# Performance work log

Measured on AMD Instinct MI355X. Metric: run time of the kernel, lower is better.

Reference implementation:

```python
import jax, jax.numpy as jnp
from jax import lax
import numpy as np
import math

NUM_CLASSES = 81
N_PER_IMG = 1024
NUM_IMAGES = 8
SCORE_THRESH = 0.05
NMS_THRESH = 0.5
DETS_PER_IMG = 100
WX, WY, WW, WH = 10.0, 10.0, 5.0, 5.0
BBOX_XFORM_CLIP = math.log(1000.0 / 16.0)


def setup_inputs() -> dict:
    key = jax.random.key(0)
    k1, k2, k3, k4 = jax.random.split(key, 4)
    M = NUM_IMAGES * N_PER_IMG
    H, W = 800, 1333
    class_logits = jax.random.normal(k1, (M, NUM_CLASSES), dtype=jnp.float32) * 3.0
    box_regression = jax.random.normal(k2, (M, 4 * NUM_CLASSES), dtype=jnp.float32) * 0.5
    # valid xyxy proposals inside the image
    xy1 = jax.random.uniform(k3, (M, 2), dtype=jnp.float32) * jnp.array([W * 0.7, H * 0.7], jnp.float32)
    wh = jax.random.uniform(k4, (M, 2), dtype=jnp.float32) * jnp.array([W * 0.3, H * 0.3], jnp.float32) + 4.0
    proposals = jnp.concatenate([xy1, xy1 + wh], axis=1)
    return {"class_logits": class_logits, "box_regression": box_regression,
            "proposals": proposals, "height": H, "width": W}


def _decode(rel_codes, boxes):
    widths = boxes[:, 2] - boxes[:, 0] + 1.0
    heights = boxes[:, 3] - boxes[:, 1] + 1.0
    ctr_x = boxes[:, 0] + 0.5 * widths
    ctr_y = boxes[:, 1] + 0.5 * heights
    rel = rel_codes.reshape(rel_codes.shape[0], -1, 4)  # [M, C, 4]
    dx = rel[:, :, 0] / WX
    dy = rel[:, :, 1] / WY
    dw = jnp.minimum(rel[:, :, 2] / WW, BBOX_XFORM_CLIP)
    dh = jnp.minimum(rel[:, :, 3] / WH, BBOX_XFORM_CLIP)
    pctr_x = dx * widths[:, None] + ctr_x[:, None]
    pctr_y = dy * heights[:, None] + ctr_y[:, None]
    pw = jnp.exp(dw) * widths[:, None]
    ph = jnp.exp(dh) * heights[:, None]
    return jnp.stack([pctr_x - 0.5 * pw, pctr_y - 0.5 * ph,
                      pctr_x + 0.5 * pw - 1.0, pctr_y + 0.5 * ph - 1.0], axis=-1)


def _clip(boxes, height, width):
    # boxes [..., 4] xyxy, clamp to [0, W-1] x [0, H-1]
    x = jnp.clip(boxes[..., 0::2], 0.0, float(width - 1))
    y = jnp.clip(boxes[..., 1::2], 0.0, float(height - 1))
    return jnp.stack([x[..., 0], y[..., 0], x[..., 1], y[..., 1]], axis=-1)


def _iou_matrix(b):
    x1, y1, x2, y2 = b[:, 0], b[:, 1], b[:, 2], b[:, 3]
    area = (x2 - x1 + 1.0) * (y2 - y1 + 1.0)
    xx1 = jnp.maximum(x1[:, None], x1[None, :])
    yy1 = jnp.maximum(y1[:, None], y1[None, :])
    xx2 = jnp.minimum(x2[:, None], x2[None, :])
    yy2 = jnp.minimum(y2[:, None], y2[None, :])
    inter = jnp.clip(xx2 - xx1 + 1.0, 0.0) * jnp.clip(yy2 - yy1 + 1.0, 0.0)
    return inter / (area[:, None] + area[None, :] - inter)


def _per_class(scores_j, boxes_j):
    # scores_j [N], boxes_j [N,4] -> sorted scores/boxes + greedy-NMS keep mask
    N = scores_j.shape[0]
    valid = scores_j > SCORE_THRESH
    s = jnp.where(valid, scores_j, 0.0)  # softmax scores are > 0
    order = jnp.argsort(-s)
    s_sorted = s[order]
    b_sorted = boxes_j[order]
    valid_sorted = valid[order]
    iou = _iou_matrix(b_sorted)  # [N, N]
    idxs = jnp.arange(N)

    def body(i, keep):
        sup = (iou[i] > NMS_THRESH) & keep[i] & (idxs > i)
        return keep & ~sup

    keep = lax.fori_loop(0, N, body, valid_sorted)
    return s_sorted, b_sorted, keep


def _per_image(prob_i, boxes_i):
    # prob_i [N, C], boxes_i [N, C, 4]; skip background class 0
    C = prob_i.shape[1]
    fg_scores = prob_i[:, 1:].T                      # [C-1, N]
    fg_boxes = jnp.swapaxes(boxes_i[:, 1:, :], 0, 1)  # [C-1, N, 4]
    s_sorted, b_sorted, keep = jax.vmap(_per_class)(fg_scores, fg_boxes)
    labels = jnp.broadcast_to(jnp.arange(1, C, dtype=jnp.int32)[:, None], s_sorted.shape)
    flat_s = jnp.where(keep, s_sorted, 0.0).reshape(-1)
    vals, idx = lax.top_k(flat_s, DETS_PER_IMG)      # detections-per-image limit
    boxes_out = b_sorted.reshape(-1, 4)[idx]
    labels_out = labels.reshape(-1)[idx]
    ok = vals > SCORE_THRESH
    return (jnp.where(ok, vals, 0.0),
            jnp.where(ok[:, None], boxes_out, 0.0),
            jnp.where(ok, labels_out, 0))


def reference(class_logits, box_regression, proposals, height, width):
    prob = jax.nn.softmax(class_logits, axis=-1)          # [M, C]
    dec = _decode(box_regression, proposals)              # [M, C, 4]
    dec = _clip(dec, height, width)
    B, N, C = NUM_IMAGES, N_PER_IMG, NUM_CLASSES
    prob = prob.reshape(B, N, C)
    dec = dec.reshape(B, N, C, 4)
    scores, boxes, labels = lax.map(lambda a: _per_image(a[0], a[1]), (prob, dec))
    return scores, boxes, labels
```

## Files before the change

### kernel.cpp

```cpp
#include <hip/hip_runtime.h>
#include <stdint.h>
#include <math.h>

#define NCLS 81
#define NFG  80
#define NPI  1024
#define NIMG 8
#define DETS 100
#define SCORE_T 0.05f
#define NMS_T   0.5f
#define NCAND   (NFG * DETS)
#define CAND_CAP 2048
#define FASTN 256
#define ROWS 64

static constexpr float BBOX_CLIP = 4.1351665567423557f;

__global__ __launch_bounds__(256) void softmax_probT(
    const float* __restrict__ logits, float* __restrict__ probT, int M)
{
    __shared__ float tile[ROWS * NCLS];
    __shared__ float mx[ROWS], dn[ROWS];
    int t = threadIdx.x;
    int rbase = blockIdx.x * ROWS;

    for (int idx = t; idx < ROWS * NCLS; idx += 256)
        tile[idx] = logits[(size_t)rbase * NCLS + idx];
    __syncthreads();

    if (t < ROWS) {
        const float* r = tile + t * NCLS;
        float m = r[0];
        #pragma unroll
        for (int j = 1; j < NCLS; ++j) m = fmaxf(m, r[j]);
        float s = 0.f;
        #pragma unroll
        for (int j = 0; j < NCLS; ++j) s += expf(r[j] - m);
        mx[t] = m; dn[t] = s;
    }
    __syncthreads();

    for (int o = t; o < ROWS * NFG; o += 256) {
        int r = o & 63;
        int c = o >> 6;
        float v = expf(tile[r * NCLS + (c + 1)] - mx[r]) / dn[r];
        probT[(size_t)c * M + rbase + r] = v;
    }
}

__global__ __launch_bounds__(256) void per_class_nms(
    const float* __restrict__ probT, const float* __restrict__ boxreg,
    const float* __restrict__ props, const int* __restrict__ hptr,
    const int* __restrict__ wptr, int* __restrict__ out_cnt,
    float* __restrict__ out_score, unsigned* __restrict__ out_key,
    float* __restrict__ out_box, int M)
{
    int pid = blockIdx.x;
    int img = pid / NFG;
    int c   = pid % NFG;
    int cls = c + 1;

    __shared__ float box_lds[NPI][4];
    __shared__ unsigned long long key[NPI];
    __shared__ int keep[NPI];
    __shared__ float sbox[FASTN][4];
    __shared__ float sarea[FASTN];
    __shared__ unsigned long long mask[FASTN][FASTN/64];
    __shared__ unsigned long long keepw[FASTN/64];
    __shared__ unsigned wpre[4];
    __shared__ int cnt;

    int t = threadIdx.x;
    float W1 = (float)(*wptr - 1);
    float H1 = (float)(*hptr - 1);

    if (t == 0) cnt = 0;
    for (int i = t; i < NPI; i += 256) key[i] = 0ULL;
    __syncthreads();

    {
        const float4 pv = *(const float4*)(probT + (size_t)c * M + img * NPI + 4 * t);
        float pr[4] = {pv.x, pv.y, pv.z, pv.w};
        #pragma unroll
        for (int j = 0; j < 4; ++j) {
            if (pr[j] > SCORE_T) {
                int m = 4 * t + j;
                int g = img * NPI + m;
                const float4 pb = *(const float4*)(props + (size_t)g * 4);
                float x1 = pb.x, y1 = pb.y, x2 = pb.z, y2 = pb.w;
                float w  = x2 - x1 + 1.0f, h = y2 - y1 + 1.0f;
                float cx = x1 + 0.5f * w,  cy = y1 + 0.5f * h;
                const float4 rc = *(const float4*)(boxreg + (size_t)g * (4 * NCLS) + 4 * cls);
                float dx = rc.x / 10.0f, dy = rc.y / 10.0f;
                float dw = fminf(rc.z / 5.0f, BBOX_CLIP);
                float dh = fminf(rc.w / 5.0f, BBOX_CLIP);
                float pcx = dx * w + cx, pcy = dy * h + cy;
                float pw = expf(dw) * w, ph = expf(dh) * h;
                float bx1 = pcx - 0.5f * pw;
                float by1 = pcy - 0.5f * ph;
                float bx2 = pcx + 0.5f * pw - 1.0f;
                float by2 = pcy + 0.5f * ph - 1.0f;
                bx1 = fminf(fmaxf(bx1, 0.f), W1);
                bx2 = fminf(fmaxf(bx2, 0.f), W1);
                by1 = fminf(fmaxf(by1, 0.f), H1);
                by2 = fminf(fmaxf(by2, 0.f), H1);
                box_lds[m][0] = bx1; box_lds[m][1] = by1;
                box_lds[m][2] = bx2; box_lds[m][3] = by2;
                int p = atomicAdd(&cnt, 1);
                unsigned fb = __float_as_uint(pr[j]);
                key[p] = ((unsigned long long)fb << 32) | (unsigned)(NPI - 1 - m);
            }
        }
    }
    __syncthreads();
    int n = cnt;

    if (n <= 64) {
        if (t < 64) {
            int lane = t;
            unsigned long long k = (lane < n) ? key[lane] : 0ULL;
            #pragma unroll
            for (int kk = 2; kk <= 64; kk <<= 1) {
                #pragma unroll
                for (int j = kk >> 1; j > 0; j >>= 1) {
                    unsigned long long o = __shfl_xor(k, j, 64);
                    bool up = ((lane & kk) == 0);
                    bool lower = ((lane & j) == 0);
                    bool take_max = (up == lower);
                    k = take_max ? (k > o ? k : o) : (k < o ? k : o);
                }
            }
            bool valid = (lane < n);
            float bx1 = 0.f, by1 = 0.f, bx2 = 0.f, by2 = 0.f, area = 0.f;
            if (valid) {
                int mi = NPI - 1 - (int)(k & 0xFFFFFFFFu);
                bx1 = box_lds[mi][0]; by1 = box_lds[mi][1];
                bx2 = box_lds[mi][2]; by2 = box_lds[mi][3];
                area = (bx2 - bx1 + 1.f) * (by2 - by1 + 1.f);
            }
            unsigned long long sup = 0ULL;
            for (int i = 0; i < n; ++i) {
                bool alive = !((sup >> i) & 1ULL);
                float ax1 = __shfl(bx1, i, 64), ay1 = __shfl(by1, i, 64);
                float ax2 = __shfl(bx2, i, 64), ay2 = __shfl(by2, i, 64);
                float aarea = __shfl(area, i, 64);
                bool s = false;
                if (alive && valid && lane > i) {
                    float xx1 = fmaxf(ax1, bx1), yy1 = fmaxf(ay1, by1);
                    float xx2 = fminf(ax2, bx2), yy2 = fminf(ay2, by2);
                    float iw = fmaxf(xx2 - xx1 + 1.f, 0.f);
                    float ih = fmaxf(yy2 - yy1 + 1.f, 0.f);
                    float inter = iw * ih;
                    float iou = inter / (aarea + area - inter);
                    s = iou > NMS_T;
                }
                sup |= __ballot(s);
            }
            bool kept = valid && !((sup >> lane) & 1ULL);
            unsigned long long keptm = __ballot(kept);
            int rank = __popcll(keptm & ((1ULL << lane) - 1ULL));
            if (kept && rank < DETS) {
                int slot = pid * DETS + rank;
                out_score[slot] = __uint_as_float((unsigned)(k >> 32));
                out_key[slot] = (unsigned)(c * NPI + lane);
                out_box[slot * 4 + 0] = bx1;
                out_box[slot * 4 + 1] = by1;
                out_box[slot * 4 + 2] = bx2;
                out_box[slot * 4 + 3] = by2;
            }
            if (lane == 0) {
                int tot = __popcll(keptm);
                out_cnt[pid] = tot < DETS ? tot : DETS;
            }
        }
        return;
    }

    int P = 2;
    while (P < n) P <<= 1;
    for (int k = 2; k <= P; k <<= 1) {
        for (int j = k >> 1; j > 0; j >>= 1) {
            for (int i = t; i < P; i += 256) {
                int ixj = i ^ j;
                if (ixj > i) {
                    unsigned long long a = key[i], b = key[ixj];
                    bool up = (i & k) == 0;
                    if (up ? (a < b) : (a > b)) { key[i] = b; key[ixj] = a; }
                }
            }
            __syncthreads();
        }
    }

    for (int i = t; i < NPI; i += 256) keep[i] = 0;
    __syncthreads();

    if (n <= FASTN) {
        for (int i = t; i < n; i += 256) {
            int mi = NPI - 1 - (int)(key[i] & 0xFFFFFFFFu);
            float bx1 = box_lds[mi][0], by1 = box_lds[mi][1];
            float bx2 = box_lds[mi][2], by2 = box_lds[mi][3];
            sbox[i][0] = bx1; sbox[i][1] = by1; sbox[i][2] = bx2; sbox[i][3] = by2;
            sarea[i] = (bx2 - bx1 + 1.f) * (by2 - by1 + 1.f);
        }
        __syncthreads();
        int nwords = ((n + 63) >> 6);
        for (int w = t; w < n * (FASTN/64); w += 256) {
            int i = w >> 2, wb = w & 3;
            if (wb >= nwords || ((wb + 1) << 6) - 1 <= i) { mask[i][wb] = 0ULL; continue; }
            float ax1 = sbox[i][0], ay1 = sbox[i][1];
            float ax2 = sbox[i][2], ay2 = sbox[i][3];
            float aarea = sarea[i];
            unsigned long long bits = 0ULL;
            int jbase = wb << 6;
            #pragma unroll 4
            for (int b = 0; b < 64; ++b) {
                int j = jbase + b;
                if (j < n && j > i) {
                    float bx1 = sbox[j][0], by1 = sbox[j][1];
                    float bx2 = sbox[j][2], by2 = sbox[j][3];
                    float xx1 = fmaxf(ax1, bx1), yy1 = fmaxf(ay1, by1);
                    float xx2 = fminf(ax2, bx2), yy2 = fminf(ay2, by2);
                    float iw = fmaxf(xx2 - xx1 + 1.f, 0.f);
                    float ih = fmaxf(yy2 - yy1 + 1.f, 0.f);
                    float inter = iw * ih;
                    float iou = inter / (aarea + sarea[j] - inter);
                    if (iou > NMS_T) bits |= (1ULL << b);
                }
            }
            mask[i][wb] = bits;
        }
        __syncthreads();
        if (t < 64) {
            int lane = t;
            unsigned long long kb = 0ULL;
            if (lane < 4) {
                int rem = n - (lane << 6);
                if (rem >= 64) kb = ~0ULL;
                else if (rem > 0) kb = (1ULL << rem) - 1ULL;
            }
            unsigned long long rm = 0ULL;
            for (int i = 0; i < n; ++i) {
                unsigned long long rw = __shfl(rm, i >> 6, 64);
                if (!((rw >> (i & 63)) & 1ULL)) {
                    unsigned long long mrow = (lane < 4) ? mask[i][lane] : 0ULL;
                    rm |= mrow;
                }
            }
            if (lane < 4) keepw[lane] = kb & ~rm;
        }
        __syncthreads();
        for (int i = t; i < n; i += 256)
            keep[i] = (int)((keepw[i >> 6] >> (i & 63)) & 1ULL);
        __syncthreads();
    } else {
        for (int i = t; i < n; i += 256) keep[i] = 1;
        __syncthreads();
        for (int i = 0; i < n; ++i) {
            if (keep[i]) {
                unsigned long long ki = key[i];
                int mi = NPI - 1 - (int)(ki & 0xFFFFFFFFu);
                float ax1 = box_lds[mi][0], ay1 = box_lds[mi][1];
                float ax2 = box_lds[mi][2], ay2 = box_lds[mi][3];
                float aarea = (ax2 - ax1 + 1.f) * (ay2 - ay1 + 1.f);
                for (int jj = i + 1 + t; jj < n; jj += 256) {
                    if (keep[jj]) {
                        int mj = NPI - 1 - (int)(key[jj] & 0xFFFFFFFFu);
                        float bx1 = box_lds[mj][0], by1 = box_lds[mj][1];
                        float bx2 = box_lds[mj][2], by2 = box_lds[mj][3];
                        float xx1 = fmaxf(ax1, bx1), yy1 = fmaxf(ay1, by1);
                        float xx2 = fminf(ax2, bx2), yy2 = fminf(ay2, by2);
                        float iw = fmaxf(xx2 - xx1 + 1.f, 0.f);
                        float ih = fmaxf(yy2 - yy1 + 1.f, 0.f);
                        float inter = iw * ih;
                        float barea = (bx2 - bx1 + 1.f) * (by2 - by1 + 1.f);
                        float iou = inter / (aarea + barea - inter);
                        if (iou > NMS_T) keep[jj] = 0;
                    }
                }
            }
            __syncthreads();
        }
    }

    {
        int lane = t & 63, w = t >> 6;
        int k0 = keep[4 * t], k1 = keep[4 * t + 1];
        int k2 = keep[4 * t + 2], k3 = keep[4 * t + 3];
        unsigned s = (unsigned)(k0 + k1 + k2 + k3);
        unsigned v = s;
        #pragma unroll
        for (int off = 1; off < 64; off <<= 1) {
            unsigned u = __shfl_up(v, off, 64);
            v += (lane >= off) ? u : 0u;
        }
        if (lane == 63) wpre[w] = v;
        __syncthreads();
        unsigned woff = 0;
        for (int w2 = 0; w2 < w; ++w2) woff += wpre[w2];
        unsigned before = v + woff - s;
        unsigned r = before;
        #pragma unroll
        for (int j = 0; j < 4; ++j) {
            int i = 4 * t + j;
            int kv = (j == 0) ? k0 : (j == 1) ? k1 : (j == 2) ? k2 : k3;
            if (kv && r < DETS) {
                unsigned long long ki = key[i];
                int mi = NPI - 1 - (int)(ki & 0xFFFFFFFFu);
                int slot = pid * DETS + (int)r;
                out_score[slot] = __uint_as_float((unsigned)(ki >> 32));
                out_key[slot] = (unsigned)(c * NPI + i);
                out_box[slot * 4 + 0] = box_lds[mi][0];
                out_box[slot * 4 + 1] = box_lds[mi][1];
                out_box[slot * 4 + 2] = box_lds[mi][2];
                out_box[slot * 4 + 3] = box_lds[mi][3];
            }
            r += (unsigned)kv;
        }
        __syncthreads();
        if (t == 0) {
            unsigned tot = wpre[0] + wpre[1] + wpre[2] + wpre[3];
            out_cnt[pid] = (int)(tot < DETS ? tot : DETS);
        }
    }
}

__device__ __forceinline__ void suffix_select(
    unsigned* hist, unsigned* wtot, int K, int* outB, unsigned* outAbove)
{
    int t = threadIdx.x, lane = t & 63, w = t >> 6;
    unsigned c0 = hist[4 * t], c1 = hist[4 * t + 1];
    unsigned c2 = hist[4 * t + 2], c3 = hist[4 * t + 3];
    unsigned ps = c0 + c1 + c2 + c3;
    unsigned v = ps;
    #pragma unroll
    for (int off = 1; off < 64; off <<= 1) {
        unsigned u = __shfl_down(v, off, 64);
        v += (lane + off < 64) ? u : 0u;
    }
    if (lane == 0) wtot[w] = v;
    __syncthreads();
    unsigned woff = 0;
    for (int w2 = w + 1; w2 < 16; ++w2) woff += wtot[w2];
    unsigned Sown = v + woff;
    unsigned A3 = Sown - ps;
    unsigned A2 = A3 + c3, A1 = A2 + c2, A0 = A1 + c1;
    unsigned A[4] = {A0, A1, A2, A3};
    unsigned C[4] = {c0, c1, c2, c3};
    #pragma unroll
    for (int j = 0; j < 4; ++j) {
        if ((int)A[j] < K && (int)(A[j] + C[j]) >= K) {
            *outB = 4 * t + j;
            *outAbove = A[j];
        }
    }
    __syncthreads();
}

__global__ __launch_bounds__(1024) void topk_merge(
    const int* __restrict__ cnts, const float* __restrict__ escore,
    const unsigned* __restrict__ ekey, const float* __restrict__ ebox,
    float* __restrict__ out)
{
    int img = blockIdx.x;
    __shared__ unsigned sc[NCAND];
    __shared__ unsigned hist[4096];
    __shared__ unsigned long long cand[CAND_CAP];
    __shared__ unsigned wtot[16];
    __shared__ int sB1, sB2, sNc;
    __shared__ unsigned sAb1, sAb2;

    int t = threadIdx.x;
    if (t == 0) { sB1 = 0; sB2 = 0; sNc = 0; sAb1 = 0; sAb2 = 0; }
    for (int p = t; p < NCAND; p += 1024) {
        int cc = p / DETS, k = p % DETS;
        unsigned fb = 0;
        if (k < cnts[img * NFG + cc]) fb = __float_as_uint(escore[img * NCAND + p]);
        sc[p] = fb;
    }
    for (int i = t; i < 4096; i += 1024) hist[i] = 0;
    __syncthreads();

    for (int p = t; p < NCAND; p += 1024) {
        unsigned fb = sc[p];
        if (fb) atomicAdd(&hist[fb >> 19], 1u);
    }
    __syncthreads();
    suffix_select(hist, wtot, DETS, &sB1, &sAb1);
    int B1 = sB1;
    unsigned ab1 = sAb1;

    for (int i = t; i < 4096; i += 1024) hist[i] = 0;
    __syncthreads();
    for (int p = t; p < NCAND; p += 1024) {
        unsigned fb = sc[p];
        if (fb && (int)(fb >> 19) == B1) atomicAdd(&hist[(fb >> 7) & 0xFFFu], 1u);
    }
    __syncthreads();
    suffix_select(hist, wtot, DETS - (int)ab1, &sB2, &sAb2);
    int B2 = sB2;

    for (int p = t; p < NCAND; p += 1024) {
        unsigned fb = sc[p];
        if (fb) {
            int d1 = (int)(fb >> 19);
            bool ok = d1 > B1 || (d1 == B1 && (int)((fb >> 7) & 0xFFFu) >= B2);
            if (ok) {
                int pos = atomicAdd(&sNc, 1);
                if (pos < CAND_CAP) {
                    unsigned fk = ekey[img * NCAND + p];
                    unsigned low = ((0x1FFFFu - fk) << 13) | (unsigned)p;
                    cand[pos] = ((unsigned long long)fb << 32) | low;
                }
            }
        }
    }
    __syncthreads();
    int nc = sNc < CAND_CAP ? sNc : CAND_CAP;
    int P = 128;
    while (P < nc) P <<= 1;
    for (int i = t; i < P; i += 1024)
        if (i >= nc) cand[i] = 0ULL;
    __syncthreads();

    for (int k = 2; k <= P; k <<= 1) {
        for (int j = k >> 1; j > 0; j >>= 1) {
            for (int i = t; i < P; i += 1024) {
                int ixj = i ^ j;
                if (ixj > i) {
                    unsigned long long a = cand[i], b = cand[ixj];
                    bool up = (i & k) == 0;
                    if (up ? (a < b) : (a > b)) { cand[i] = b; cand[ixj] = a; }
                }
            }
            __syncthreads();
        }
    }

    float* oScore = out;
    float* oBox   = out + NIMG * DETS;
    float* oLab   = out + NIMG * DETS * 5;

    if (t < DETS) {
        unsigned long long b = cand[t];
        int o = img * DETS + t;
        if (b != 0ULL) {
            float scv = __uint_as_float((unsigned)(b >> 32));
            unsigned low = (unsigned)(b & 0xFFFFFFFFu);
            unsigned flatkey = 0x1FFFFu - ((low >> 13) & 0x1FFFFu);
            int p = (int)(low & 0x1FFFu);
            int gp = img * NCAND + p;
            oScore[o] = scv;
            oBox[o * 4 + 0] = ebox[gp * 4 + 0];
            oBox[o * 4 + 1] = ebox[gp * 4 + 1];
            oBox[o * 4 + 2] = ebox[gp * 4 + 2];
            oBox[o * 4 + 3] = ebox[gp * 4 + 3];
            oLab[o] = (float)((flatkey >> 10) + 1);
        } else {
            oScore[o] = 0.f;
            oBox[o * 4 + 0] = 0.f; oBox[o * 4 + 1] = 0.f;
            oBox[o * 4 + 2] = 0.f; oBox[o * 4 + 3] = 0.f;
            oLab[o] = 0.f;
        }
    }
}

extern "C" void kernel_launch(void* const* d_in, const int* in_sizes, int n_in,
                              void* d_out, int out_size, void* d_ws, size_t ws_size,
                              hipStream_t stream) {
    const float* logits = (const float*)d_in[0];
    const float* boxreg = (const float*)d_in[1];
    const float* props  = (const float*)d_in[2];
    const int*   hptr   = (const int*)d_in[3];
    const int*   wptr   = (const int*)d_in[4];
    float* out = (float*)d_out;
    int M = in_sizes[0] / NCLS;

    char* ws = (char*)d_ws;
    float*    probT  = (float*)ws;    ws += (size_t)NFG * M * sizeof(float);
    int*      cnt    = (int*)ws;      ws += (size_t)NIMG * NFG * sizeof(int);
    float*    escore = (float*)ws;    ws += (size_t)NIMG * NCAND * sizeof(float);
    unsigned* ekey   = (unsigned*)ws; ws += (size_t)NIMG * NCAND * sizeof(unsigned);
    float*    ebox   = (float*)ws;    ws += (size_t)NIMG * NCAND * 4 * sizeof(float);

    softmax_probT<<<M / ROWS, 256, 0, stream>>>(logits, probT, M);
    per_class_nms<<<NIMG * NFG, 256, 0, stream>>>(
        probT, boxreg, props, hptr, wptr, cnt, escore, ekey, ebox, M);
    topk_merge<<<NIMG, 1024, 0, stream>>>(cnt, escore, ekey, ebox, out);
}
```

Before: 61.07 us.

## Fuse top-k merge into NMS kernel via last-block completion counter

Replaces the transposed probability materialization with a per-row max/denominator stats kernel, so the NMS kernel computes class probabilities directly from the logits. The separate top-k merge launch is folded into the NMS kernel: the last block to finish each image, detected with an atomic counter, performs the merge in 256 threads using shared memory unioned with the NMS buffers. This removes one launch and the probT write and read, at the cost of strided logit reads, a serial tail where one 256-thread block merges each image, and reliance on the stats kernel resetting the done counters.

```diff
diff --git a/kernel.cpp b/kernel.cpp
--- a/kernel.cpp
+++ b/kernel.cpp
@@ -16,433 +16,123 @@
 
 static constexpr float BBOX_CLIP = 4.1351665567423557f;
 
-__global__ __launch_bounds__(256) void softmax_probT(
-    const float* __restrict__ logits, float* __restrict__ probT, int M)
+struct ShP2 {
+    float box[NPI][4];
+    unsigned long long key[NPI];
+    int keep[NPI];
+    float sbox[FASTN][4];
+    float sarea[FASTN];
+    unsigned long long mask[FASTN][FASTN/64];
+    unsigned long long keepw[FASTN/64];
+    unsigned wpre[4];
+};
+struct ShP3 {
+    unsigned hist[4096];
+    unsigned long long cand[CAND_CAP];
+    int cnts[NFG];
+    unsigned wtot[4];
+    int B1, B2, Nc;
+    unsigned Ab1, Ab2;
+};
+union ShU { ShP2 p2; ShP3 p3; };
+
+__device__ __forceinline__ void suffix_select256(
+    unsigned* hist, unsigned* wtot, int K, int* outB, unsigned* outAbove)
 {
-    __shared__ float tile[ROWS * NCLS];
-    __shared__ float mx[ROWS], dn[ROWS];
+    int t = threadIdx.x, lane = t & 63, w = t >> 6;
+    unsigned loc[16]; unsigned ps = 0;
+    #pragma unroll
+    for (int j = 0; j < 16; ++j) { loc[j] = hist[t * 16 + j]; ps += loc[j]; }
+    unsigned v = ps;
+    #pragma unroll
+    for (int off = 1; off < 64; off <<= 1) {
+        unsigned u = __shfl_down(v, off, 64);
+        v += (lane + off < 64) ? u : 0u;
+    }
+    if (lane == 0) wtot[w] = v;
+    __syncthreads();
+    unsigned woff = 0;
+    for (int w2 = w + 1; w2 < 4; ++w2) woff += wtot[w2];
+    unsigned base = v + woff - ps;
+    unsigned suf = 0;
+    #pragma unroll
+    for (int j = 15; j >= 0; --j) {
+        unsigned A = base + suf;
+        if ((int)A < K && (int)(A + loc[j]) >= K) { *outB = t * 16 + j; *outAbove = A; }
+        suf += loc[j];
+    }
+    __syncthreads();
+}
+
+__device__ void merge_image(
+    int img, ShP3& s3, const int* gcnt, const float* escore,
+    const unsigned* ekey, const float* ebox, float* out)
+{
     int t = threadIdx.x;
-    int rbase = blockIdx.x * ROWS;
-
-    for (int idx = t; idx < ROWS * NCLS; idx += 256)
-        tile[idx] = logits[(size_t)rbase * NCLS + idx];
-    __syncthreads();
-
-    if (t < ROWS) {
-        const float* r = tile + t * NCLS;
-        float m = r[0];
-        #pragma unroll
-        for (int j = 1; j < NCLS; ++j) m = fmaxf(m, r[j]);
-        float s = 0.f;
-        #pragma unroll
-        for (int j = 0; j < NCLS; ++j) s += expf(r[j] - m);
-        mx[t] = m; dn[t] = s;
-    }
-    __syncthreads();
-
-    for (int o = t; o < ROWS * NFG; o += 256) {
-        int r = o & 63;
-        int c = o >> 6;
-        float v = expf(tile[r * NCLS + (c + 1)] - mx[r]) / dn[r];
-        probT[(size_t)c * M + rbase + r] = v;
-    }
-}
-
-__global__ __launch_bounds__(256) void per_class_nms(
-    const float* __restrict__ probT, const float* __restrict__ boxreg,
-    const float* __restrict__ props, const int* __restrict__ hptr,
-    const int* __restrict__ wptr, int* __restrict__ out_cnt,
-    float* __restrict__ out_score, unsigned* __restrict__ out_key,
-    float* __restrict__ out_box, int M)
-{
-    int pid = blockIdx.x;
-    int img = pid / NFG;
-    int c   = pid % NFG;
-    int cls = c + 1;
-
-    __shared__ float box_lds[NPI][4];
-    __shared__ unsigned long long key[NPI];
-    __shared__ int keep[NPI];
-    __shared__ float sbox[FASTN][4];
-    __shared__ float sarea[FASTN];
-    __shared__ unsigned long long mask[FASTN][FASTN/64];
-    __shared__ unsigned long long keepw[FASTN/64];
-    __shared__ unsigned wpre[4];
-    __shared__ int cnt;
-
-    int t = threadIdx.x;
-    float W1 = (float)(*wptr - 1);
-    float H1 = (float)(*hptr - 1);
-
-    if (t == 0) cnt = 0;
-    for (int i = t; i < NPI; i += 256) key[i] = 0ULL;
-    __syncthreads();
-
-    {
-        const float4 pv = *(const float4*)(probT + (size_t)c * M + img * NPI + 4 * t);
-        float pr[4] = {pv.x, pv.y, pv.z, pv.w};
-        #pragma unroll
-        for (int j = 0; j < 4; ++j) {
-            if (pr[j] > SCORE_T) {
-                int m = 4 * t + j;
-                int g = img * NPI + m;
-                const float4 pb = *(const float4*)(props + (size_t)g * 4);
-                float x1 = pb.x, y1 = pb.y, x2 = pb.z, y2 = pb.w;
-                float w  = x2 - x1 + 1.0f, h = y2 - y1 + 1.0f;
-                float cx = x1 + 0.5f * w,  cy = y1 + 0.5f * h;
-                const float4 rc = *(const float4*)(boxreg + (size_t)g * (4 * NCLS) + 4 * cls);
-                float dx = rc.x / 10.0f, dy = rc.y / 10.0f;
-                float dw = fminf(rc.z / 5.0f, BBOX_CLIP);
-                float dh = fminf(rc.w / 5.0f, BBOX_CLIP);
-                float pcx = dx * w + cx, pcy = dy * h + cy;
-                float pw = expf(dw) * w, ph = expf(dh) * h;
-                float bx1 = pcx - 0.5f * pw;
-                float by1 = pcy - 0.5f * ph;
-                float bx2 = pcx + 0.5f * pw - 1.0f;
-                float by2 = pcy + 0.5f * ph - 1.0f;
-                bx1 = fminf(fmaxf(bx1, 0.f), W1);
-                bx2 = fminf(fmaxf(bx2, 0.f), W1);
-                by1 = fminf(fmaxf(by1, 0.f), H1);
-                by2 = fminf(fmaxf(by2, 0.f), H1);
-                box_lds[m][0] = bx1; box_lds[m][1] = by1;
-                box_lds[m][2] = bx2; box_lds[m][3] = by2;
-                int p = atomicAdd(&cnt, 1);
-                unsigned fb = __float_as_uint(pr[j]);
-                key[p] = ((unsigned long long)fb << 32) | (unsigned)(NPI - 1 - m);
-            }
-        }
-    }
-    __syncthreads();
-    int n = cnt;
-
-    if (n <= 64) {
-        if (t < 64) {
-            int lane = t;
-            unsigned long long k = (lane < n) ? key[lane] : 0ULL;
-            #pragma unroll
-            for (int kk = 2; kk <= 64; kk <<= 1) {
-                #pragma unroll
-                for (int j = kk >> 1; j > 0; j >>= 1) {
-                    unsigned long long o = __shfl_xor(k, j, 64);
-                    bool up = ((lane & kk) == 0);
-                    bool lower = ((lane & j) == 0);
-                    bool take_max = (up == lower);
-                    k = take_max ? (k > o ? k : o) : (k < o ? k : o);
-                }
-            }
-            bool valid = (lane < n);
-            float bx1 = 0.f, by1 = 0.f, bx2 = 0.f, by2 = 0.f, area = 0.f;
-            if (valid) {
-                int mi = NPI - 1 - (int)(k & 0xFFFFFFFFu);
-                bx1 = box_lds[mi][0]; by1 = box_lds[mi][1];
-                bx2 = box_lds[mi][2]; by2 = box_lds[mi][3];
-                area = (bx2 - bx1 + 1.f) * (by2 - by1 + 1.f);
-            }
-            unsigned long long sup = 0ULL;
-            for (int i = 0; i < n; ++i) {
-                bool alive = !((sup >> i) & 1ULL);
-                float ax1 = __shfl(bx1, i, 64), ay1 = __shfl(by1, i, 64);
-                float ax2 = __shfl(bx2, i, 64), ay2 = __shfl(by2, i, 64);
-                float aarea = __shfl(area, i, 64);
-                bool s = false;
-                if (alive && valid && lane > i) {
-                    float xx1 = fmaxf(ax1, bx1), yy1 = fmaxf(ay1, by1);
-                    float xx2 = fminf(ax2, bx2), yy2 = fminf(ay2, by2);
-                    float iw = fmaxf(xx2 - xx1 + 1.f, 0.f);
-                    float ih = fmaxf(yy2 - yy1 + 1.f, 0.f);
-                    float inter = iw * ih;
-                    float iou = inter / (aarea + area - inter);
-                    s = iou > NMS_T;
-                }
-                sup |= __ballot(s);
-            }
-            bool kept = valid && !((sup >> lane) & 1ULL);
-            unsigned long long keptm = __ballot(kept);
-            int rank = __popcll(keptm & ((1ULL << lane) - 1ULL));
-            if (kept && rank < DETS) {
-                int slot = pid * DETS + rank;
-                out_score[slot] = __uint_as_float((unsigned)(k >> 32));
-                out_key[slot] = (unsigned)(c * NPI + lane);
-                out_box[slot * 4 + 0] = bx1;
-                out_box[slot * 4 + 1] = by1;
-                out_box[slot * 4 + 2] = bx2;
-                out_box[slot * 4 + 3] = by2;
-            }
-            if (lane == 0) {
-                int tot = __popcll(keptm);
-                out_cnt[pid] = tot < DETS ? tot : DETS;
-            }
-        }
-        return;
-    }
-
-    int P = 2;
-    while (P < n) P <<= 1;
+    if (t < NFG) s3.cnts[t] = gcnt[img * NFG + t];
+    if (t == 0) { s3.B1 = 0; s3.B2 = 0; s3.Nc = 0; s3.Ab1 = 0; s3.Ab2 = 0; }
+    for (int i = t; i < 4096; i += 256) s3.hist[i] = 0;
+    __syncthreads();
+    for (int p = t; p < NCAND; p += 256) {
+        if ((p % DETS) < s3.cnts[p / DETS]) {
+            unsigned fb = __float_as_uint(escore[img * NCAND + p]);
+            atomicAdd(&s3.hist[fb >> 19], 1u);
+        }
+    }
+    __syncthreads();
+    suffix_select256(s3.hist, s3.wtot, DETS, &s3.B1, &s3.Ab1);
+    int B1 = s3.B1; unsigned ab1 = s3.Ab1;
+    for (int i = t; i < 4096; i += 256) s3.hist[i] = 0;
+    __syncthreads();
+    for (int p = t; p < NCAND; p += 256) {
+        if ((p % DETS) < s3.cnts[p / DETS]) {
+            unsigned fb = __float_as_uint(escore[img * NCAND + p]);
+            if ((int)(fb >> 19) == B1) atomicAdd(&s3.hist[(fb >> 7) & 0xFFFu], 1u);
+        }
+    }
+    __syncthreads();
+    suffix_select256(s3.hist, s3.wtot, DETS - (int)ab1, &s3.B2, &s3.Ab2);
+    int B2 = s3.B2;
+    for (int p = t; p < NCAND; p += 256) {
+        if ((p % DETS) < s3.cnts[p / DETS]) {
+            unsigned fb = __float_as_uint(escore[img * NCAND + p]);
+            int d1 = (int)(fb >> 19);
+            bool ok = d1 > B1 || (d1 == B1 && (int)((fb >> 7) & 0xFFFu) >= B2);
+            if (ok) {
+                int pos = atomicAdd(&s3.Nc, 1);
+                if (pos < CAND_CAP) {
+                    unsigned fk = ekey[img * NCAND + p];
+                    s3.cand[pos] = ((unsigned long long)fb << 32)
+                                 | (((0x1FFFFu - fk) << 13) | (unsigned)p);
+                }
+            }
+        }
+    }
+    __syncthreads();
+    int nc = s3.Nc < CAND_CAP ? s3.Nc : CAND_CAP;
+    int P = 128;
+    while (P < nc) P <<= 1;
+    for (int i = t; i < P; i += 256)
+        if (i >= nc) s3.cand[i] = 0ULL;
+    __syncthreads();
     for (int k = 2; k <= P; k <<= 1) {
         for (int j = k >> 1; j > 0; j >>= 1) {
             for (int i = t; i < P; i += 256) {
                 int ixj = i ^ j;
                 if (ixj > i) {
-                    unsigned long long a = key[i], b = key[ixj];
+                    unsigned long long a = s3.cand[i], b = s3.cand[ixj];
                     bool up = (i & k) == 0;
-                    if (up ? (a < b) : (a > b)) { key[i] = b; key[ixj] = a; }
-                }
-            }
-            __syncthreads();
-        }
-    }
-
-    for (int i = t; i < NPI; i += 256) keep[i] = 0;
-    __syncthreads();
-
-    if (n <= FASTN) {
-        for (int i = t; i < n; i += 256) {
-            int mi = NPI - 1 - (int)(key[i] & 0xFFFFFFFFu);
-            float bx1 = box_lds[mi][0], by1 = box_lds[mi][1];
-            float bx2 = box_lds[mi][2], by2 = box_lds[mi][3];
-            sbox[i][0] = bx1; sbox[i][1] = by1; sbox[i][2] = bx2; sbox[i][3] = by2;
-            sarea[i] = (bx2 - bx1 + 1.f) * (by2 - by1 + 1.f);
-        }
-        __syncthreads();
-        int nwords = ((n + 63) >> 6);
-        for (int w = t; w < n * (FASTN/64); w += 256) {
-            int i = w >> 2, wb = w & 3;
-            if (wb >= nwords || ((wb + 1) << 6) - 1 <= i) { mask[i][wb] = 0ULL; continue; }
-            float ax1 = sbox[i][0], ay1 = sbox[i][1];
-            float ax2 = sbox[i][2], ay2 = sbox[i][3];
-            float aarea = sarea[i];
-            unsigned long long bits = 0ULL;
-            int jbase = wb << 6;
-            #pragma unroll 4
-            for (int b = 0; b < 64; ++b) {
-                int j = jbase + b;
-                if (j < n && j > i) {
-                    float bx1 = sbox[j][0], by1 = sbox[j][1];
-                    float bx2 = sbox[j][2], by2 = sbox[j][3];
-                    float xx1 = fmaxf(ax1, bx1), yy1 = fmaxf(ay1, by1);
-                    float xx2 = fminf(ax2, bx2), yy2 = fminf(ay2, by2);
-                    float iw = fmaxf(xx2 - xx1 + 1.f, 0.f);
-                    float ih = fmaxf(yy2 - yy1 + 1.f, 0.f);
-                    float inter = iw * ih;
-                    float iou = inter / (aarea + sarea[j] - inter);
-                    if (iou > NMS_T) bits |= (1ULL << b);
-                }
-            }
-            mask[i][wb] = bits;
-        }
-        __syncthreads();
-        if (t < 64) {
-            int lane = t;
-            unsigned long long kb = 0ULL;
-            if (lane < 4) {
-                int rem = n - (lane << 6);
-                if (rem >= 64) kb = ~0ULL;
-                else if (rem > 0) kb = (1ULL << rem) - 1ULL;
-            }
-            unsigned long long rm = 0ULL;
-            for (int i = 0; i < n; ++i) {
-                unsigned long long rw = __shfl(rm, i >> 6, 64);
-                if (!((rw >> (i & 63)) & 1ULL)) {
-                    unsigned long long mrow = (lane < 4) ? mask[i][lane] : 0ULL;
-                    rm |= mrow;
-                }
-            }
-            if (lane < 4) keepw[lane] = kb & ~rm;
-        }
-        __syncthreads();
-        for (int i = t; i < n; i += 256)
-            keep[i] = (int)((keepw[i >> 6] >> (i & 63)) & 1ULL);
-        __syncthreads();
-    } else {
-        for (int i = t; i < n; i += 256) keep[i] = 1;
-        __syncthreads();
-        for (int i = 0; i < n; ++i) {
-            if (keep[i]) {
-                unsigned long long ki = key[i];
-                int mi = NPI - 1 - (int)(ki & 0xFFFFFFFFu);
-                float ax1 = box_lds[mi][0], ay1 = box_lds[mi][1];
-                float ax2 = box_lds[mi][2], ay2 = box_lds[mi][3];
-                float aarea = (ax2 - ax1 + 1.f) * (ay2 - ay1 + 1.f);
-                for (int jj = i + 1 + t; jj < n; jj += 256) {
-                    if (keep[jj]) {
-                        int mj = NPI - 1 - (int)(key[jj] & 0xFFFFFFFFu);
-                        float bx1 = box_lds[mj][0], by1 = box_lds[mj][1];
-                        float bx2 = box_lds[mj][2], by2 = box_lds[mj][3];
-                        float xx1 = fmaxf(ax1, bx1), yy1 = fmaxf(ay1, by1);
-                        float xx2 = fminf(ax2, bx2), yy2 = fminf(ay2, by2);
-                        float iw = fmaxf(xx2 - xx1 + 1.f, 0.f);
-                        float ih = fmaxf(yy2 - yy1 + 1.f, 0.f);
-                        float inter = iw * ih;
-                        float barea = (bx2 - bx1 + 1.f) * (by2 - by1 + 1.f);
-                        float iou = inter / (aarea + barea - inter);
-                        if (iou > NMS_T) keep[jj] = 0;
-                    }
-                }
-            }
-            __syncthreads();
-        }
-    }
-
-    {
-        int lane = t & 63, w = t >> 6;
-        int k0 = keep[4 * t], k1 = keep[4 * t + 1];
-        int k2 = keep[4 * t + 2], k3 = keep[4 * t + 3];
-        unsigned s = (unsigned)(k0 + k1 + k2 + k3);
-        unsigned v = s;
-        #pragma unroll
-        for (int off = 1; off < 64; off <<= 1) {
-            unsigned u = __shfl_up(v, off, 64);
-            v += (lane >= off) ? u : 0u;
-        }
-        if (lane == 63) wpre[w] = v;
-        __syncthreads();
-        unsigned woff = 0;
-        for (int w2 = 0; w2 < w; ++w2) woff += wpre[w2];
-        unsigned before = v + woff - s;
-        unsigned r = before;
-        #pragma unroll
-        for (int j = 0; j < 4; ++j) {
-            int i = 4 * t + j;
-            int kv = (j == 0) ? k0 : (j == 1) ? k1 : (j == 2) ? k2 : k3;
-            if (kv && r < DETS) {
-                unsigned long long ki = key[i];
-                int mi = NPI - 1 - (int)(ki & 0xFFFFFFFFu);
-                int slot = pid * DETS + (int)r;
-                out_score[slot] = __uint_as_float((unsigned)(ki >> 32));
-                out_key[slot] = (unsigned)(c * NPI + i);
-                out_box[slot * 4 + 0] = box_lds[mi][0];
-                out_box[slot * 4 + 1] = box_lds[mi][1];
-                out_box[slot * 4 + 2] = box_lds[mi][2];
-                out_box[slot * 4 + 3] = box_lds[mi][3];
-            }
-            r += (unsigned)kv;
-        }
-        __syncthreads();
-        if (t == 0) {
-            unsigned tot = wpre[0] + wpre[1] + wpre[2] + wpre[3];
-            out_cnt[pid] = (int)(tot < DETS ? tot : DETS);
-        }
-    }
-}
-
-__device__ __forceinline__ void suffix_select(
-    unsigned* hist, unsigned* wtot, int K, int* outB, unsigned* outAbove)
-{
-    int t = threadIdx.x, lane = t & 63, w = t >> 6;
-    unsigned c0 = hist[4 * t], c1 = hist[4 * t + 1];
-    unsigned c2 = hist[4 * t + 2], c3 = hist[4 * t + 3];
-    unsigned ps = c0 + c1 + c2 + c3;
-    unsigned v = ps;
-    #pragma unroll
-    for (int off = 1; off < 64; off <<= 1) {
-        unsigned u = __shfl_down(v, off, 64);
-        v += (lane + off < 64) ? u : 0u;
-    }
-    if (lane == 0) wtot[w] = v;
-    __syncthreads();
-    unsigned woff = 0;
-    for (int w2 = w + 1; w2 < 16; ++w2) woff += wtot[w2];
-    unsigned Sown = v + woff;
-    unsigned A3 = Sown - ps;
-    unsigned A2 = A3 + c3, A1 = A2 + c2, A0 = A1 + c1;
-    unsigned A[4] = {A0, A1, A2, A3};
-    unsigned C[4] = {c0, c1, c2, c3};
-    #pragma unroll
-    for (int j = 0; j < 4; ++j) {
-        if ((int)A[j] < K && (int)(A[j] + C[j]) >= K) {
-            *outB = 4 * t + j;
-            *outAbove = A[j];
-        }
-    }
-    __syncthreads();
-}
-
-__global__ __launch_bounds__(1024) void topk_merge(
-    const int* __restrict__ cnts, const float* __restrict__ escore,
-    const unsigned* __restrict__ ekey, const float* __restrict__ ebox,
-    float* __restrict__ out)
-{
-    int img = blockIdx.x;
-    __shared__ unsigned sc[NCAND];
-    __shared__ unsigned hist[4096];
-    __shared__ unsigned long long cand[CAND_CAP];
-    __shared__ unsigned wtot[16];
-    __shared__ int sB1, sB2, sNc;
-    __shared__ unsigned sAb1, sAb2;
-
-    int t = threadIdx.x;
-    if (t == 0) { sB1 = 0; sB2 = 0; sNc = 0; sAb1 = 0; sAb2 = 0; }
-    for (int p = t; p < NCAND; p += 1024) {
-        int cc = p / DETS, k = p % DETS;
-        unsigned fb = 0;
-        if (k < cnts[img * NFG + cc]) fb = __float_as_uint(escore[img * NCAND + p]);
-        sc[p] = fb;
-    }
-    for (int i = t; i < 4096; i += 1024) hist[i] = 0;
-    __syncthreads();
-
-    for (int p = t; p < NCAND; p += 1024) {
-        unsigned fb = sc[p];
-        if (fb) atomicAdd(&hist[fb >> 19], 1u);
-    }
-    __syncthreads();
-    suffix_select(hist, wtot, DETS, &sB1, &sAb1);
-    int B1 = sB1;
-    unsigned ab1 = sAb1;
-
-    for (int i = t; i < 4096; i += 1024) hist[i] = 0;
-    __syncthreads();
-    for (int p = t; p < NCAND; p += 1024) {
-        unsigned fb = sc[p];
-        if (fb && (int)(fb >> 19) == B1) atomicAdd(&hist[(fb >> 7) & 0xFFFu], 1u);
-    }
-    __syncthreads();
-    suffix_select(hist, wtot, DETS - (int)ab1, &sB2, &sAb2);
-    int B2 = sB2;
-
-    for (int p = t; p < NCAND; p += 1024) {
-        unsigned fb = sc[p];
-        if (fb) {
-            int d1 = (int)(fb >> 19);
-            bool ok = d1 > B1 || (d1 == B1 && (int)((fb >> 7) & 0xFFFu) >= B2);
-            if (ok) {
-                int pos = atomicAdd(&sNc, 1);
-                if (pos < CAND_CAP) {
-                    unsigned fk = ekey[img * NCAND + p];
-                    unsigned low = ((0x1FFFFu - fk) << 13) | (unsigned)p;
-                    cand[pos] = ((unsigned long long)fb << 32) | low;
-                }
-            }
-        }
-    }
-    __syncthreads();
-    int nc = sNc < CAND_CAP ? sNc : CAND_CAP;
-    int P = 128;
-    while (P < nc) P <<= 1;
-    for (int i = t; i < P; i += 1024)
-        if (i >= nc) cand[i] = 0ULL;
-    __syncthreads();
-
-    for (int k = 2; k <= P; k <<= 1) {
-        for (int j = k >> 1; j > 0; j >>= 1) {
-            for (int i = t; i < P; i += 1024) {
-                int ixj = i ^ j;
-                if (ixj > i) {
-                    unsigned long long a = cand[i], b = cand[ixj];
-                    bool up = (i & k) == 0;
-                    if (up ? (a < b) : (a > b)) { cand[i] = b; cand[ixj] = a; }
-                }
-            }
-            __syncthreads();
-        }
-    }
-
+                    if (up ? (a < b) : (a > b)) { s3.cand[i] = b; s3.cand[ixj] = a; }
+                }
+            }
+            __syncthreads();
+        }
+    }
     float* oScore = out;
     float* oBox   = out + NIMG * DETS;
     float* oLab   = out + NIMG * DETS * 5;
-
     if (t < DETS) {
-        unsigned long long b = cand[t];
+        unsigned long long b = s3.cand[t];
         int o = img * DETS + t;
         if (b != 0ULL) {
             float scv = __uint_as_float((unsigned)(b >> 32));
@@ -465,6 +155,299 @@
     }
 }
 
+__global__ __launch_bounds__(256) void row_stats(
+    const float* __restrict__ logits, float* __restrict__ mxout,
+    float* __restrict__ dnout, int* __restrict__ done, int M)
+{
+    __shared__ float tile[ROWS * NCLS];
+    int t = threadIdx.x;
+    int rbase = blockIdx.x * ROWS;
+    if (blockIdx.x == 0 && t < NIMG) done[t] = 0;
+    for (int idx = t; idx < ROWS * NCLS; idx += 256)
+        tile[idx] = logits[(size_t)rbase * NCLS + idx];
+    __syncthreads();
+    if (t < ROWS) {
+        const float* r = tile + t * NCLS;
+        float m = r[0];
+        #pragma unroll
+        for (int j = 1; j < NCLS; ++j) m = fmaxf(m, r[j]);
+        float s = 0.f;
+        #pragma unroll
+        for (int j = 0; j < NCLS; ++j) s += expf(r[j] - m);
+        mxout[rbase + t] = m;
+        dnout[rbase + t] = s;
+    }
+}
+
+__global__ __launch_bounds__(256) void nms_merge(
+    const float* __restrict__ logits, const float* __restrict__ boxreg,
+    const float* __restrict__ props, const int* __restrict__ hptr,
+    const int* __restrict__ wptr, const float* __restrict__ mxin,
+    const float* __restrict__ dnin, int* done, int* gcnt,
+    float* escore, unsigned* ekey, float* ebox,
+    float* __restrict__ out, int M)
+{
+    int pid = blockIdx.x;
+    int img = pid / NFG;
+    int c   = pid % NFG;
+    int cls = c + 1;
+
+    __shared__ ShU sh;
+    __shared__ int cnt;
+    __shared__ int lastflag;
+    int t = threadIdx.x;
+    float W1 = (float)(*wptr - 1);
+    float H1 = (float)(*hptr - 1);
+
+    if (t == 0) cnt = 0;
+    for (int i = t; i < NPI; i += 256) sh.p2.key[i] = 0ULL;
+    __syncthreads();
+
+    {
+        const float4 mxv = *(const float4*)(mxin + img * NPI + 4 * t);
+        const float4 dnv = *(const float4*)(dnin + img * NPI + 4 * t);
+        float mxa[4] = {mxv.x, mxv.y, mxv.z, mxv.w};
+        float dna[4] = {dnv.x, dnv.y, dnv.z, dnv.w};
+        #pragma unroll
+        for (int j = 0; j < 4; ++j) {
+            int m = 4 * t + j;
+            int g = img * NPI + m;
+            float pr = expf(logits[(size_t)g * NCLS + cls] - mxa[j]) / dna[j];
+            if (pr > SCORE_T) {
+                const float4 pb = *(const float4*)(props + (size_t)g * 4);
+                float x1 = pb.x, y1 = pb.y, x2 = pb.z, y2 = pb.w;
+                float w  = x2 - x1 + 1.0f, h = y2 - y1 + 1.0f;
+                float cx = x1 + 0.5f * w,  cy = y1 + 0.5f * h;
+                const float4 rc = *(const float4*)(boxreg + (size_t)g * (4 * NCLS) + 4 * cls);
+                float dx = rc.x / 10.0f, dy = rc.y / 10.0f;
+                float dw = fminf(rc.z / 5.0f, BBOX_CLIP);
+                float dh = fminf(rc.w / 5.0f, BBOX_CLIP);
+                float pcx = dx * w + cx, pcy = dy * h + cy;
+                float pw = expf(dw) * w, ph = expf(dh) * h;
+                float bx1 = fminf(fmaxf(pcx - 0.5f * pw, 0.f), W1);
+                float by1 = fminf(fmaxf(pcy - 0.5f * ph, 0.f), H1);
+                float bx2 = fminf(fmaxf(pcx + 0.5f * pw - 1.0f, 0.f), W1);
+                float by2 = fminf(fmaxf(pcy + 0.5f * ph - 1.0f, 0.f), H1);
+                sh.p2.box[m][0] = bx1; sh.p2.box[m][1] = by1;
+                sh.p2.box[m][2] = bx2; sh.p2.box[m][3] = by2;
+                int p = atomicAdd(&cnt, 1);
+                sh.p2.key[p] = ((unsigned long long)__float_as_uint(pr) << 32)
+                             | (unsigned)(NPI - 1 - m);
+            }
+        }
+    }
+    __syncthreads();
+    int n = cnt;
+
+    if (n <= 64) {
+        if (t < 64) {
+            int lane = t;
+            unsigned long long k = (lane < n) ? sh.p2.key[lane] : 0ULL;
+            #pragma unroll
+            for (int kk = 2; kk <= 64; kk <<= 1) {
+                #pragma unroll
+                for (int j = kk >> 1; j > 0; j >>= 1) {
+                    unsigned long long o = __shfl_xor(k, j, 64);
+                    bool take_max = (((lane & kk) == 0) == ((lane & j) == 0));
+                    k = take_max ? (k > o ? k : o) : (k < o ? k : o);
+                }
+            }
+            bool valid = (lane < n);
+            float bx1 = 0.f, by1 = 0.f, bx2 = 0.f, by2 = 0.f, area = 0.f;
+            if (valid) {
+                int mi = NPI - 1 - (int)(k & 0xFFFFFFFFu);
+                bx1 = sh.p2.box[mi][0]; by1 = sh.p2.box[mi][1];
+                bx2 = sh.p2.box[mi][2]; by2 = sh.p2.box[mi][3];
+                area = (bx2 - bx1 + 1.f) * (by2 - by1 + 1.f);
+            }
+            unsigned long long sup = 0ULL;
+            for (int i = 0; i < n; ++i) {
+                bool alive = !((sup >> i) & 1ULL);
+                float ax1 = __shfl(bx1, i, 64), ay1 = __shfl(by1, i, 64);
+                float ax2 = __shfl(bx2, i, 64), ay2 = __shfl(by2, i, 64);
+                float aarea = __shfl(area, i, 64);
+                bool s = false;
+                if (alive && valid && lane > i) {
+                    float xx1 = fmaxf(ax1, bx1), yy1 = fmaxf(ay1, by1);
+                    float xx2 = fminf(ax2, bx2), yy2 = fminf(ay2, by2);
+                    float iw = fmaxf(xx2 - xx1 + 1.f, 0.f);
+                    float ih = fmaxf(yy2 - yy1 + 1.f, 0.f);
+                    float inter = iw * ih;
+                    s = inter / (aarea + area - inter) > NMS_T;
+                }
+                sup |= __ballot(s);
+            }
+            bool kept = valid && !((sup >> lane) & 1ULL);
+            unsigned long long keptm = __ballot(kept);
+            int rank = __popcll(keptm & ((1ULL << lane) - 1ULL));
+            if (kept && rank < DETS) {
+                int slot = pid * DETS + rank;
+                escore[slot] = __uint_as_float((unsigned)(k >> 32));
+                ekey[slot] = (unsigned)(c * NPI + lane);
+                ebox[slot * 4 + 0] = bx1; ebox[slot * 4 + 1] = by1;
+                ebox[slot * 4 + 2] = bx2; ebox[slot * 4 + 3] = by2;
+            }
+            if (lane == 0) {
+                int tot = __popcll(keptm);
+                gcnt[pid] = tot < DETS ? tot : DETS;
+            }
+        }
+    } else {
+        int P = 2;
+        while (P < n) P <<= 1;
+        for (int k = 2; k <= P; k <<= 1) {
+            for (int j = k >> 1; j > 0; j >>= 1) {
+                for (int i = t; i < P; i += 256) {
+                    int ixj = i ^ j;
+                    if (ixj > i) {
+                        unsigned long long a = sh.p2.key[i], b = sh.p2.key[ixj];
+                        bool up = (i & k) == 0;
+                        if (up ? (a < b) : (a > b)) { sh.p2.key[i] = b; sh.p2.key[ixj] = a; }
+                    }
+                }
+                __syncthreads();
+            }
+        }
+        for (int i = t; i < NPI; i += 256) sh.p2.keep[i] = 0;
+        __syncthreads();
+
+        if (n <= FASTN) {
+            for (int i = t; i < n; i += 256) {
+                int mi = NPI - 1 - (int)(sh.p2.key[i] & 0xFFFFFFFFu);
+                float bx1 = sh.p2.box[mi][0], by1 = sh.p2.box[mi][1];
+                float bx2 = sh.p2.box[mi][2], by2 = sh.p2.box[mi][3];
+                sh.p2.sbox[i][0] = bx1; sh.p2.sbox[i][1] = by1;
+                sh.p2.sbox[i][2] = bx2; sh.p2.sbox[i][3] = by2;
+                sh.p2.sarea[i] = (bx2 - bx1 + 1.f) * (by2 - by1 + 1.f);
+            }
+            __syncthreads();
+            int nwords = ((n + 63) >> 6);
+            for (int w = t; w < n * (FASTN/64); w += 256) {
+                int i = w >> 2, wb = w & 3;
+                if (wb >= nwords || ((wb + 1) << 6) - 1 <= i) { sh.p2.mask[i][wb] = 0ULL; continue; }
+                float ax1 = sh.p2.sbox[i][0], ay1 = sh.p2.sbox[i][1];
+                float ax2 = sh.p2.sbox[i][2], ay2 = sh.p2.sbox[i][3];
+                float aarea = sh.p2.sarea[i];
+                unsigned long long bits = 0ULL;
+                int jbase = wb << 6;
+                #pragma unroll 4
+                for (int b = 0; b < 64; ++b) {
+                    int j = jbase + b;
+                    if (j < n && j > i) {
+                        float bx1 = sh.p2.sbox[j][0], by1 = sh.p2.sbox[j][1];
+                        float bx2 = sh.p2.sbox[j][2], by2 = sh.p2.sbox[j][3];
+                        float xx1 = fmaxf(ax1, bx1), yy1 = fmaxf(ay1, by1);
+                        float xx2 = fminf(ax2, bx2), yy2 = fminf(ay2, by2);
+                        float iw = fmaxf(xx2 - xx1 + 1.f, 0.f);
+                        float ih = fmaxf(yy2 - yy1 + 1.f, 0.f);
+                        float inter = iw * ih;
+                        if (inter / (aarea + sh.p2.sarea[j] - inter) > NMS_T) bits |= (1ULL << b);
+                    }
+                }
+                sh.p2.mask[i][wb] = bits;
+            }
+            __syncthreads();
+            if (t < 64) {
+                int lane = t;
+                unsigned long long kb = 0ULL;
+                if (lane < 4) {
+                    int rem = n - (lane << 6);
+                    if (rem >= 64) kb = ~0ULL;
+                    else if (rem > 0) kb = (1ULL << rem) - 1ULL;
+                }
+                unsigned long long rm = 0ULL;
+                for (int i = 0; i < n; ++i) {
+                    unsigned long long rw = __shfl(rm, i >> 6, 64);
+                    if (!((rw >> (i & 63)) & 1ULL)) {
+                        unsigned long long mrow = (lane < 4) ? sh.p2.mask[i][lane] : 0ULL;
+                        rm |= mrow;
+                    }
+                }
+                if (lane < 4) sh.p2.keepw[lane] = kb & ~rm;
+            }
+            __syncthreads();
+            for (int i = t; i < n; i += 256)
+                sh.p2.keep[i] = (int)((sh.p2.keepw[i >> 6] >> (i & 63)) & 1ULL);
+            __syncthreads();
+        } else {
+            for (int i = t; i < n; i += 256) sh.p2.keep[i] = 1;
+            __syncthreads();
+            for (int i = 0; i < n; ++i) {
+                if (sh.p2.keep[i]) {
+                    unsigned long long ki = sh.p2.key[i];
+                    int mi = NPI - 1 - (int)(ki & 0xFFFFFFFFu);
+                    float ax1 = sh.p2.box[mi][0], ay1 = sh.p2.box[mi][1];
+                    float ax2 = sh.p2.box[mi][2], ay2 = sh.p2.box[mi][3];
+                    float aarea = (ax2 - ax1 + 1.f) * (ay2 - ay1 + 1.f);
+                    for (int jj = i + 1 + t; jj < n; jj += 256) {
+                        if (sh.p2.keep[jj]) {
+                            int mj = NPI - 1 - (int)(sh.p2.key[jj] & 0xFFFFFFFFu);
+                            float bx1 = sh.p2.box[mj][0], by1 = sh.p2.box[mj][1];
+                            float bx2 = sh.p2.box[mj][2], by2 = sh.p2.box[mj][3];
+                            float xx1 = fmaxf(ax1, bx1), yy1 = fmaxf(ay1, by1);
+                            float xx2 = fminf(ax2, bx2), yy2 = fminf(ay2, by2);
+                            float iw = fmaxf(xx2 - xx1 + 1.f, 0.f);
+                            float ih = fmaxf(yy2 - yy1 + 1.f, 0.f);
+                            float inter = iw * ih;
+                            float barea = (bx2 - bx1 + 1.f) * (by2 - by1 + 1.f);
+                            if (inter / (aarea + barea - inter) > NMS_T) sh.p2.keep[jj] = 0;
+                        }
+                    }
+                }
+                __syncthreads();
+            }
+        }
+        {
+            int lane = t & 63, w = t >> 6;
+            int k0 = sh.p2.keep[4 * t], k1 = sh.p2.keep[4 * t + 1];
+            int k2 = sh.p2.keep[4 * t + 2], k3 = sh.p2.keep[4 * t + 3];
+            unsigned s = (unsigned)(k0 + k1 + k2 + k3);
+            unsigned v = s;
+            #pragma unroll
+            for (int off = 1; off < 64; off <<= 1) {
+                unsigned u = __shfl_up(v, off, 64);
+                v += (lane >= off) ? u : 0u;
+            }
+            if (lane == 63) sh.p2.wpre[w] = v;
+            __syncthreads();
+            unsigned woff = 0;
+            for (int w2 = 0; w2 < w; ++w2) woff += sh.p2.wpre[w2];
+            unsigned r = v + woff - s;
+            #pragma unroll
+            for (int j = 0; j < 4; ++j) {
+                int i = 4 * t + j;
+                int kv = (j == 0) ? k0 : (j == 1) ? k1 : (j == 2) ? k2 : k3;
+                if (kv && r < DETS) {
+                    unsigned long long ki = sh.p2.key[i];
+                    int mi = NPI - 1 - (int)(ki & 0xFFFFFFFFu);
+                    int slot = pid * DETS + (int)r;
+                    escore[slot] = __uint_as_float((unsigned)(ki >> 32));
+                    ekey[slot] = (unsigned)(c * NPI + i);
+                    ebox[slot * 4 + 0] = sh.p2.box[mi][0];
+                    ebox[slot * 4 + 1] = sh.p2.box[mi][1];
+                    ebox[slot * 4 + 2] = sh.p2.box[mi][2];
+                    ebox[slot * 4 + 3] = sh.p2.box[mi][3];
+                }
+                r += (unsigned)kv;
+            }
+            __syncthreads();
+            if (t == 0) {
+                unsigned tot = sh.p2.wpre[0] + sh.p2.wpre[1] + sh.p2.wpre[2] + sh.p2.wpre[3];
+                gcnt[pid] = (int)(tot < DETS ? tot : DETS);
+            }
+        }
+    }
+
+    __threadfence();
+    __syncthreads();
+    if (t == 0) lastflag = (atomicAdd(&done[img], 1) == NFG - 1);
+    __syncthreads();
+    if (lastflag) {
+        __threadfence();
+        merge_image(img, sh.p3, gcnt, escore, ekey, ebox, out);
+    }
+}
+
 extern "C" void kernel_launch(void* const* d_in, const int* in_sizes, int n_in,
                               void* d_out, int out_size, void* d_ws, size_t ws_size,
                               hipStream_t stream) {
@@ -477,14 +460,16 @@
     int M = in_sizes[0] / NCLS;
 
     char* ws = (char*)d_ws;
-    float*    probT  = (float*)ws;    ws += (size_t)NFG * M * sizeof(float);
-    int*      cnt    = (int*)ws;      ws += (size_t)NIMG * NFG * sizeof(int);
+    float*    mx     = (float*)ws;    ws += (size_t)M * sizeof(float);
+    float*    den    = (float*)ws;    ws += (size_t)M * sizeof(float);
+    int*      done   = (int*)ws;      ws += (size_t)NIMG * sizeof(int) + 32;
+    int*      gcnt   = (int*)ws;      ws += (size_t)NIMG * NFG * sizeof(int);
     float*    escore = (float*)ws;    ws += (size_t)NIMG * NCAND * sizeof(float);
     unsigned* ekey   = (unsigned*)ws; ws += (size_t)NIMG * NCAND * sizeof(unsigned);
     float*    ebox   = (float*)ws;    ws += (size_t)NIMG * NCAND * 4 * sizeof(float);
 
-    softmax_probT<<<M / ROWS, 256, 0, stream>>>(logits, probT, M);
-    per_class_nms<<<NIMG * NFG, 256, 0, stream>>>(
-        probT, boxreg, props, hptr, wptr, cnt, escore, ekey, ebox, M);
-    topk_merge<<<NIMG, 1024, 0, stream>>>(cnt, escore, ekey, ebox, out);
+    row_stats<<<M / ROWS, 256, 0, stream>>>(logits, mx, den, done, M);
+    nms_merge<<<NIMG * NFG, 256, 0, stream>>>(
+        logits, boxreg, props, hptr, wptr, mx, den, done, gcnt,
+        escore, ekey, ebox, out, M);
 }
```

Measured after the change: 105.8 us. +73.3%, slower.
